# Performance work log

Hardware: AMD Instinct MI355X
Metric: run time of the kernel (lower is better)

The kernel has to match this reference:

```python
import jax, jax.numpy as jnp
import numpy as np

N = 100000      # nodes
E = 1600000     # directed edges
F_IN = 128      # node feature dim
H = 128         # hidden dim
C = 16          # classes


def setup_inputs() -> dict:
    key = jax.random.key(0)
    ks = jax.random.split(key, 8)
    s = 1.0 / np.sqrt(H)
    return {
        "x": jax.random.normal(ks[0], (N, F_IN), dtype=jnp.float32),
        "edge_index": jax.random.randint(ks[1], (2, E), 0, N, dtype=jnp.int32),
        "W1": jax.random.normal(ks[2], (F_IN, H), dtype=jnp.float32) * s,
        "b1": jnp.zeros((H,), jnp.float32),
        "W2": jax.random.normal(ks[3], (H, H), dtype=jnp.float32) * s,
        "b2": jnp.zeros((H,), jnp.float32),
        "W3": jax.random.normal(ks[4], (H, H), dtype=jnp.float32) * s,
        "b3": jnp.zeros((H,), jnp.float32),
        "Wfc": jax.random.normal(ks[5], (H, C), dtype=jnp.float32) * s,
        "bfc": jnp.zeros((C,), jnp.float32),
    }


def _gcn_conv(x, W, b, src, dst, norm):
    # x' = b + scatter_add over edges of norm * (x @ W)[src] into dst
    h = x @ W                                   # [N, H] dense GEMM
    msg = h[src] * norm[:, None]                # [E+N, H] gather + scale
    out = jax.ops.segment_sum(msg, dst, num_segments=N)  # scatter-add
    return out + b


def reference(x, edge_index, W1, b1, W2, b2, W3, b3, Wfc, bfc):
    loops = jnp.arange(N, dtype=edge_index.dtype)
    src = jnp.concatenate([edge_index[0], loops])   # [E+N] with self-loops
    dst = jnp.concatenate([edge_index[1], loops])
    # symmetric normalization deg^{-1/2}[src] * deg^{-1/2}[dst] (PyG default)
    deg = jax.ops.segment_sum(jnp.ones_like(dst, dtype=x.dtype), dst, num_segments=N)
    dinv = jax.lax.rsqrt(deg)                       # deg >= 1 due to self-loops
    norm = dinv[src] * dinv[dst]

    h = jax.nn.elu(_gcn_conv(x, W1, b1, src, dst, norm))   # dropout is identity in eval
    h = jax.nn.elu(_gcn_conv(h, W2, b2, src, dst, norm))
    h = jax.nn.elu(_gcn_conv(h, W3, b3, src, dst, norm))
    logits = h @ Wfc + bfc                                  # [N, C]
    return jax.nn.log_softmax(logits, axis=-1)
```

## Files before the change

kernel.cpp:

```cpp
#include <hip/hip_runtime.h>
#include <math.h>

#define HDIM 128
#define CDIM 16
#define CAP 48
#define ASTR 136
#define HSTR 132
#define NBINS 256
#define TILE 4096
#define F2SPLIT 4

typedef unsigned short u16;
typedef unsigned int u32;
typedef __attribute__((ext_vector_type(8))) short short8;
typedef __attribute__((ext_vector_type(4))) float f32x4;
typedef __attribute__((ext_vector_type(2))) float f32x2;

__device__ inline u16 f2bf(float f) {
  u32 u = __float_as_uint(f);
  u += 0x7fffu + ((u >> 16) & 1u);
  return (u16)(u >> 16);
}
__device__ inline float bf_lo(u32 p) { return __uint_as_float(p << 16); }
__device__ inline float bf_hi(u32 p) { return __uint_as_float(p & 0xffff0000u); }
__device__ inline u32 pack2(float a, float b) {
  return (u32)f2bf(a) | ((u32)f2bf(b) << 16);
}
__device__ inline u32 cvtpk(float a, float b) {
  u32 r;
  asm("v_cvt_pk_bf16_f32 %0, %1, %2" : "=v"(r) : "v"(a), "v"(b));
  return r;
}
__device__ inline void acc_word(f32x2& acc, u32 w) {
  f32x2 x;
  x.x = __uint_as_float(w << 16);
  x.y = __uint_as_float(w & 0xffff0000u);
  asm("v_pk_add_f32 %0, %1, %2" : "=v"(acc) : "v"(x), "v"(acc));
}


__global__ __launch_bounds__(256) void bin_kernel(const int* __restrict__ ei,
                                                  int* __restrict__ cursor,
                                                  int2* __restrict__ bins,
                                                  int binCap, int E, int npb, int nbE,
                                                  int* __restrict__ deg, int N,
                                                  const float* __restrict__ W0,
                                                  const float* __restrict__ W1,
                                                  const float* __restrict__ W2,
                                                  u16* __restrict__ Wt) {
  int tid = threadIdx.x;
  if (blockIdx.x >= nbE) {
    int t = (blockIdx.x - nbE) * 256 + tid;
    int which = t >> 14, idx = t & 16383;
    int n = idx >> 7, k = idx & 127;
    const float* W = which == 0 ? W0 : (which == 1 ? W1 : W2);
    Wt[(size_t)which * HDIM * HDIM + n * HDIM + k] = f2bf(W[k * HDIM + n]);
    return;
  }
  {
    int i = blockIdx.x * 256 + tid;
    if (i < N) deg[i] = 0;
  }
  __shared__ int2 eds[TILE];
  __shared__ int base[NBINS], rank[NBINS], hist[NBINS];
  int t0 = blockIdx.x * TILE;
  int n = min(TILE, E - t0);
  for (int i = tid; i < NBINS; i += 256) { hist[i] = 0; rank[i] = 0; }
  __syncthreads();
  for (int i = tid; i < n; i += 256) {
    int s = ei[t0 + i];
    int d = ei[E + t0 + i];
    eds[i] = make_int2(d, s);
    atomicAdd(&hist[d / npb], 1);
  }
  __syncthreads();
  for (int i = tid; i < NBINS; i += 256) {
    int h = hist[i];
    base[i] = h ? atomicAdd(&cursor[i], h) : 0;
  }
  __syncthreads();
  for (int i = tid; i < n; i += 256) {
    int2 e = eds[i];
    int b = e.x / npb;
    int r = base[b] + atomicAdd(&rank[b], 1);
    if (r < binCap) bins[(size_t)b * binCap + r] = e;
  }
}

__global__ __launch_bounds__(256) void fill2_kernel(const int2* __restrict__ bins,
                                                    const int* __restrict__ cursor,
                                                    int binCap, int* __restrict__ deg,
                                                    int* __restrict__ csr) {
  int b = blockIdx.x & (NBINS - 1);
  int part = blockIdx.x >> 8;
  int cnt = min(cursor[b], binCap);
  const int2* eb = bins + (size_t)b * binCap;
  for (int i = part * 256 + threadIdx.x; i < cnt; i += 256 * F2SPLIT) {
    int2 e = eb[i];
    int p = atomicAdd(&deg[e.x], 1);
    if (p < CAP) csr[(size_t)e.x * CAP + p] = e.y;
  }
}

__global__ __launch_bounds__(256) void pad_kernel(const int* __restrict__ deg,
                                                  int* __restrict__ csr, int N) {
  int n = blockIdx.x * 256 + threadIdx.x;
  if (n >= N) return;
  int d = min(deg[n], CAP);
  int dp = (d + 7) & ~7;
  int* row = csr + (size_t)n * CAP;
  for (int i = d; i < dp; ++i) row[i] = N;
}


template <bool FP32IN>
__global__ __launch_bounds__(256) void gemm_k(const void* __restrict__ Xv,
                                              const u16* __restrict__ Wt,
                                              const int* __restrict__ deg,
                                              u16* __restrict__ G, int N) {
  __shared__ u16 As[64 * ASTR];
  __shared__ u16 Wsm[128 * ASTR];
  int tid = threadIdx.x;
  int row0 = blockIdx.x * 64;

  {
    int r = tid >> 2, c = tid & 3;
    int rg = row0 + r;
    if (rg >= N) rg = N - 1;
    uint4* dst = (uint4*)(As + r * ASTR + c * 32);
    if (FP32IN) {
      const float4* src = (const float4*)((const float*)Xv + (size_t)rg * HDIM + c * 32);
#pragma unroll
      for (int j = 0; j < 4; ++j) {
        float4 a = src[2 * j], b = src[2 * j + 1];
        uint4 o;
        o.x = pack2(a.x, a.y); o.y = pack2(a.z, a.w);
        o.z = pack2(b.x, b.y); o.w = pack2(b.z, b.w);
        dst[j] = o;
      }
    } else {
      const uint4* src = (const uint4*)((const u16*)Xv + (size_t)rg * HDIM + c * 32);
      dst[0] = src[0]; dst[1] = src[1]; dst[2] = src[2]; dst[3] = src[3];
    }
  }
  {
    int r = tid >> 1, h = tid & 1;
    const uint4* src = (const uint4*)(Wt + r * HDIM + h * 64);
    uint4* dst = (uint4*)(Wsm + r * ASTR + h * 64);
#pragma unroll
    for (int i = 0; i < 8; ++i) dst[i] = src[i];
  }
  __syncthreads();

  int w = tid >> 6;
  int l = tid & 63;
  int m = l & 15, q = l >> 4;

  f32x4 acc[8];
#pragma unroll
  for (int i = 0; i < 8; ++i) acc[i] = (f32x4){0.f, 0.f, 0.f, 0.f};

#pragma unroll
  for (int kc = 0; kc < 4; ++kc) {
    short8 af = *(const short8*)(As + (w * 16 + m) * ASTR + kc * 32 + q * 8);
#pragma unroll
    for (int nt = 0; nt < 8; ++nt) {
      short8 bfr = *(const short8*)(Wsm + (nt * 16 + m) * ASTR + kc * 32 + q * 8);
      acc[nt] = __builtin_amdgcn_mfma_f32_16x16x32_bf16(af, bfr, acc[nt], 0, 0, 0);
    }
  }
  __syncthreads();

  float dv[4];
#pragma unroll
  for (int r = 0; r < 4; ++r) {
    int rg = row0 + w * 16 + q * 4 + r;
    dv[r] = rsqrtf((float)(deg[rg < N ? rg : N - 1] + 1));
  }
#pragma unroll
  for (int nt = 0; nt < 8; ++nt)
#pragma unroll
    for (int r = 0; r < 4; ++r)
      As[(w * 16 + q * 4 + r) * ASTR + nt * 16 + m] = f2bf(acc[nt][r] * dv[r]);
  __syncthreads();

  {
    int r = tid >> 2, c = tid & 3;
    int rg = row0 + r;
    if (rg < N) {
      uint4* dst = (uint4*)(G + (size_t)rg * HDIM + c * 32);
      const uint4* src = (const uint4*)(As + r * ASTR + c * 32);
      dst[0] = src[0]; dst[1] = src[1]; dst[2] = src[2]; dst[3] = src[3];
    }
  }
}


__device__ inline void gather16(const u16* __restrict__ G, const int* __restrict__ deg,
                                const int* __restrict__ csr,
                                const float4* __restrict__ b4, int node, int l, float* v) {
  const char* Gb = (const char*)G;
  f32x2 p0, p1, p2, p3;
  {
    uint4 sr = *(const uint4*)(Gb + ((size_t)node << 8) + (l << 4));
    p0.x = bf_lo(sr.x); p0.y = bf_hi(sr.x);
    p1.x = bf_lo(sr.y); p1.y = bf_hi(sr.y);
    p2.x = bf_lo(sr.z); p2.y = bf_hi(sr.z);
    p3.x = bf_lo(sr.w); p3.y = bf_hi(sr.w);
  }
  int dfull = deg[node];
  int d = min(dfull, CAP);
  int dp = (d + 7) & ~7;
  const int* row = csr + (size_t)node * CAP;
  int i0 = row[l];
  int i1 = d > 16 ? row[16 + l] : 0;
  int i2 = d > 32 ? row[32 + l] : 0;

#define GLD(u) (*(const uint4*)(Gb + (((u32)(u)) << 8) + (l << 4)))
#define AW(gv) { acc_word(p0, gv.x); acc_word(p1, gv.y); acc_word(p2, gv.z); acc_word(p3, gv.w); }
  for (int k = 0; k < dp; k += 8) {
    int s = k < 16 ? i0 : (k < 32 ? i1 : i2);
    int bl = k & 15;
    int u0 = __shfl(s, bl + 0, 16), u1 = __shfl(s, bl + 1, 16);
    int u2 = __shfl(s, bl + 2, 16), u3 = __shfl(s, bl + 3, 16);
    int u4 = __shfl(s, bl + 4, 16), u5 = __shfl(s, bl + 5, 16);
    int u6 = __shfl(s, bl + 6, 16), u7 = __shfl(s, bl + 7, 16);
    uint4 g0 = GLD(u0), g1 = GLD(u1), g2 = GLD(u2), g3 = GLD(u3);
    uint4 g4 = GLD(u4), g5 = GLD(u5), g6 = GLD(u6), g7 = GLD(u7);
    AW(g0) AW(g1) AW(g2) AW(g3) AW(g4) AW(g5) AW(g6) AW(g7)
  }
#undef AW
#undef GLD
  float dvn = rsqrtf((float)(dfull + 1));
  float4 b0 = b4[l * 2], b1 = b4[l * 2 + 1];
  v[0] = fmaf(dvn, p0.x, b0.x); v[1] = fmaf(dvn, p0.y, b0.y);
  v[2] = fmaf(dvn, p1.x, b0.z); v[3] = fmaf(dvn, p1.y, b0.w);
  v[4] = fmaf(dvn, p2.x, b1.x); v[5] = fmaf(dvn, p2.y, b1.y);
  v[6] = fmaf(dvn, p3.x, b1.z); v[7] = fmaf(dvn, p3.y, b1.w);
#pragma unroll
  for (int j = 0; j < 8; ++j) v[j] = v[j] > 0.f ? v[j] : __expf(v[j]) - 1.f;
}


__global__ __launch_bounds__(256) void agg_bf(const u16* __restrict__ G,
                                              const int* __restrict__ deg,
                                              const int* __restrict__ csr,
                                              const float* __restrict__ b,
                                              u16* __restrict__ out, int N) {
  int node = blockIdx.x * 16 + (threadIdx.x >> 4);
  if (node >= N) return;
  int l = threadIdx.x & 15;
  float v[8];
  gather16(G, deg, csr, (const float4*)b, node, l, v);
  uint4 o;
  o.x = cvtpk(v[0], v[1]); o.y = cvtpk(v[2], v[3]);
  o.z = cvtpk(v[4], v[5]); o.w = cvtpk(v[6], v[7]);
  *(uint4*)(out + (size_t)node * HDIM + l * 8) = o;
}


__global__ __launch_bounds__(256) void agg_fc(const u16* __restrict__ G,
                                              const int* __restrict__ deg,
                                              const int* __restrict__ csr,
                                              const float* __restrict__ b,
                                              const float* __restrict__ Wfc,
                                              const float* __restrict__ bfc,
                                              float* __restrict__ out, int N) {
  __shared__ float Hs[16 * HSTR];
  __shared__ float Wl[HDIM * CDIM];
  int tid = threadIdx.x;
  for (int i = tid; i < HDIM * CDIM; i += 256) Wl[i] = Wfc[i];

  int node0 = blockIdx.x * 16;
  int lr = tid >> 4, l = tid & 15;
  int node = node0 + lr;
  if (node < N) {
    float v[8];
    gather16(G, deg, csr, (const float4*)b, node, l, v);
    float4* dst = (float4*)(Hs + lr * HSTR + l * 8);
    dst[0] = make_float4(v[0], v[1], v[2], v[3]);
    dst[1] = make_float4(v[4], v[5], v[6], v[7]);
  }
  __syncthreads();

  int rg = node0 + lr;
  if (rg >= N) return;
  int c = l;
  const float* hrow = Hs + lr * HSTR;
  float acc = bfc[c];
#pragma unroll 4
  for (int k4 = 0; k4 < 32; ++k4) {
    float4 g = *(const float4*)(hrow + k4 * 4);
    const float* wk = Wl + (k4 * 4) * CDIM + c;
    acc = fmaf(g.x, wk[0 * CDIM], acc);
    acc = fmaf(g.y, wk[1 * CDIM], acc);
    acc = fmaf(g.z, wk[2 * CDIM], acc);
    acc = fmaf(g.w, wk[3 * CDIM], acc);
  }
  float mx = acc;
  for (int off = 8; off >= 1; off >>= 1) mx = fmaxf(mx, __shfl_xor(mx, off, 16));
  float ex = __expf(acc - mx);
  float ssum = ex;
  for (int off = 8; off >= 1; off >>= 1) ssum += __shfl_xor(ssum, off, 16);
  out[(size_t)rg * CDIM + c] = (acc - mx) - __logf(ssum);
}


extern "C" void kernel_launch(void* const* d_in, const int* in_sizes, int n_in,
                              void* d_out, int out_size, void* d_ws, size_t ws_size,
                              hipStream_t stream) {
  const float* x   = (const float*)d_in[0];
  const int*   ei  = (const int*)d_in[1];
  const float* W1  = (const float*)d_in[2];
  const float* b1  = (const float*)d_in[3];
  const float* W2  = (const float*)d_in[4];
  const float* b2  = (const float*)d_in[5];
  const float* W3  = (const float*)d_in[6];
  const float* b3  = (const float*)d_in[7];
  const float* Wfc = (const float*)d_in[8];
  const float* bfc = (const float*)d_in[9];

  const int N = in_sizes[0] / HDIM;
  const int E = in_sizes[1] / 2;
  const int npb = (N + NBINS - 1) / NBINS;
  const int binCap = (E + NBINS - 1) / NBINS + 1024;
  const int nbE = (E + TILE - 1) / TILE;
  const int nbW = 3 * HDIM * HDIM / 256;

  char* ws = (char*)d_ws;
  size_t off = 0;
  auto alloc = [&](size_t bytes) -> void* {
    void* p = ws + off;
    off += (bytes + 511) & ~(size_t)511;
    return p;
  };
  int*   deg    = (int*)alloc((size_t)N * 4);
  int*   cursor = (int*)alloc((size_t)NBINS * 4);
  int*   csr    = (int*)alloc((size_t)N * CAP * 4);
  int2*  bins   = (int2*)alloc((size_t)NBINS * binCap * 8);
  u16*   Wt     = (u16*)alloc((size_t)3 * HDIM * HDIM * 2);
  u16*   A      = (u16*)alloc((size_t)(N + 1) * HDIM * 2);
  u16*   B      = (u16*)alloc((size_t)(N + 1) * HDIM * 2);

  hipMemsetAsync(cursor, 0, (size_t)NBINS * 4, stream);
  hipMemsetAsync(A + (size_t)N * HDIM, 0, HDIM * 2, stream);
  hipMemsetAsync(B + (size_t)N * HDIM, 0, HDIM * 2, stream);
  bin_kernel<<<nbE + nbW, 256, 0, stream>>>(ei, cursor, bins, binCap, E, npb, nbE, deg, N, W1,
                                            W2, W3, Wt);
  fill2_kernel<<<NBINS * F2SPLIT, 256, 0, stream>>>(bins, cursor, binCap, deg, csr);
  pad_kernel<<<(N + 255) / 256, 256, 0, stream>>>(deg, csr, N);

  int grid64 = (N + 63) / 64;
  int grid16 = (N + 15) / 16;
  gemm_k<true><<<grid64, 256, 0, stream>>>(x, Wt, deg, A, N);
  agg_bf<<<grid16, 256, 0, stream>>>(A, deg, csr, b1, B, N);
  gemm_k<false><<<grid64, 256, 0, stream>>>(B, Wt + HDIM * HDIM, deg, A, N);
  agg_bf<<<grid16, 256, 0, stream>>>(A, deg, csr, b2, B, N);
  gemm_k<false><<<grid64, 256, 0, stream>>>(B, Wt + 2 * HDIM * HDIM, deg, A, N);
  agg_fc<<<grid16, 256, 0, stream>>>(A, deg, csr, b3, Wfc, bfc, (float*)d_out, N);
}
```

Measured before the change: 406.9 us.

## Fuse neighbor aggregation with the next layer's GEMM in one kernel

The separate aggregation kernel and the following dense GEMM kernel are replaced by a single kernel. Each block gathers 16 nodes' aggregated features into shared memory, multiplies them by the next weight matrix with bf16 MFMA, pre-scales the result by deg^-1/2, and writes the bf16 output. This removes a full write and read of an N×128 intermediate and two kernel launches per fused layer. In exchange, each block reads the weight matrix straight from global memory with only a 16-row tile, which could reduce GEMM efficiency.

```diff
diff --git a/kernel.cpp b/kernel.cpp
--- a/kernel.cpp
+++ b/kernel.cpp
@@ -242,20 +242,61 @@
 }
 
 
-__global__ __launch_bounds__(256) void agg_bf(const u16* __restrict__ G,
-                                              const int* __restrict__ deg,
-                                              const int* __restrict__ csr,
-                                              const float* __restrict__ b,
-                                              u16* __restrict__ out, int N) {
-  int node = blockIdx.x * 16 + (threadIdx.x >> 4);
-  if (node >= N) return;
-  int l = threadIdx.x & 15;
-  float v[8];
-  gather16(G, deg, csr, (const float4*)b, node, l, v);
-  uint4 o;
-  o.x = cvtpk(v[0], v[1]); o.y = cvtpk(v[2], v[3]);
-  o.z = cvtpk(v[4], v[5]); o.w = cvtpk(v[6], v[7]);
-  *(uint4*)(out + (size_t)node * HDIM + l * 8) = o;
+__global__ __launch_bounds__(256) void agg_gemm(const u16* __restrict__ G,
+                                                const int* __restrict__ deg,
+                                                const int* __restrict__ csr,
+                                                const float* __restrict__ b,
+                                                const u16* __restrict__ Wn,
+                                                u16* __restrict__ Gout, int N) {
+  __shared__ u16 As[16 * ASTR];
+  __shared__ float dvs[16];
+  int tid = threadIdx.x;
+  int node0 = blockIdx.x * 16;
+  int lr = tid >> 4, l = tid & 15;
+  int node = node0 + lr;
+  if (tid < 16) dvs[tid] = rsqrtf((float)(deg[min(node0 + tid, N - 1)] + 1));
+  if (node < N) {
+    float v[8];
+    gather16(G, deg, csr, (const float4*)b, node, l, v);
+    uint4 o;
+    o.x = cvtpk(v[0], v[1]); o.y = cvtpk(v[2], v[3]);
+    o.z = cvtpk(v[4], v[5]); o.w = cvtpk(v[6], v[7]);
+    *(uint4*)(As + lr * ASTR + l * 8) = o;
+  } else {
+    uint4 z = make_uint4(0, 0, 0, 0);
+    *(uint4*)(As + lr * ASTR + l * 8) = z;
+  }
+  __syncthreads();
+
+  int w = tid >> 6;
+  int lw = tid & 63;
+  int m = lw & 15, q = lw >> 4;
+  f32x4 acc0 = (f32x4){0.f, 0.f, 0.f, 0.f};
+  f32x4 acc1 = (f32x4){0.f, 0.f, 0.f, 0.f};
+#pragma unroll
+  for (int kc = 0; kc < 4; ++kc) {
+    short8 af = *(const short8*)(As + m * ASTR + kc * 32 + q * 8);
+    short8 b0 = *(const short8*)(Wn + ((w * 2 + 0) * 16 + m) * HDIM + kc * 32 + q * 8);
+    short8 b1 = *(const short8*)(Wn + ((w * 2 + 1) * 16 + m) * HDIM + kc * 32 + q * 8);
+    acc0 = __builtin_amdgcn_mfma_f32_16x16x32_bf16(af, b0, acc0, 0, 0, 0);
+    acc1 = __builtin_amdgcn_mfma_f32_16x16x32_bf16(af, b1, acc1, 0, 0, 0);
+  }
+  __syncthreads();
+
+#pragma unroll
+  for (int r = 0; r < 4; ++r) {
+    float dvr = dvs[q * 4 + r];
+    As[(q * 4 + r) * ASTR + (w * 2 + 0) * 16 + m] = f2bf(acc0[r] * dvr);
+    As[(q * 4 + r) * ASTR + (w * 2 + 1) * 16 + m] = f2bf(acc1[r] * dvr);
+  }
+  __syncthreads();
+
+  {
+    int r = tid >> 4, c = tid & 15;
+    if (node0 + r < N)
+      *(uint4*)(Gout + (size_t)(node0 + r) * HDIM + c * 8) =
+          *(const uint4*)(As + r * ASTR + c * 8);
+  }
 }
 
 
@@ -353,9 +394,7 @@
   int grid64 = (N + 63) / 64;
   int grid16 = (N + 15) / 16;
   gemm_k<true><<<grid64, 256, 0, stream>>>(x, Wt, deg, A, N);
-  agg_bf<<<grid16, 256, 0, stream>>>(A, deg, csr, b1, B, N);
-  gemm_k<false><<<grid64, 256, 0, stream>>>(B, Wt + HDIM * HDIM, deg, A, N);
-  agg_bf<<<grid16, 256, 0, stream>>>(A, deg, csr, b2, B, N);
-  gemm_k<false><<<grid64, 256, 0, stream>>>(B, Wt + 2 * HDIM * HDIM, deg, A, N);
+  agg_gemm<<<grid16, 256, 0, stream>>>(A, deg, csr, b1, Wt + HDIM * HDIM, B, N);
+  agg_gemm<<<grid16, 256, 0, stream>>>(B, deg, csr, b2, Wt + 2 * HDIM * HDIM, A, N);
   agg_fc<<<grid16, 256, 0, stream>>>(A, deg, csr, b3, Wfc, bfc, (float*)d_out, N);
 }
```

Result: faster. 383.0 us (-5.9%).
